# Kernel optimization log

Measured on AMD Instinct MI355X. Metric: run time of the kernel, lower is better.

The kernel has to match this reference:

```python
import jax, jax.numpy as jnp
import numpy as np
from jax import lax

EPS = 1e-10
NUM_ITERATIONS = 3  # init arg num_iterations
M, R = 16384, 32


def setup_inputs() -> dict:
    key = jax.random.key(0)
    x = jax.random.normal(key, (M, R, 2), dtype=jnp.float32)
    return {"x": x}


def reference(x):
    # x: (M, R, 2) -> complex (M, R); work with QT (R, M) so rows = columns
    r = x.shape[1]
    xc = (x[..., 0] + 1j * x[..., 1]).T  # (R, M) complex64
    idx = jnp.arange(r)

    # --- classical Gram-Schmidt pass (sequential over columns j) ---
    def gs_col(QT, j):
        def proj(v, i):
            qi = QT[i]
            coeff = jnp.sum(jnp.conj(qi) * v) * (i < j)  # only previous cols
            return v - coeff * qi, None
        v, _ = lax.scan(proj, xc[j], idx)
        v = v / jnp.sqrt(jnp.sum(jnp.abs(v) ** 2) + EPS)
        return QT.at[j].set(v), None

    QT, _ = lax.scan(gs_col, jnp.zeros_like(xc), idx)

    # --- iterative refinement sweeps: each column uses the OLD Q -> vmap over j ---
    def refine_col(QT, j):
        def proj(v, i):
            qi = QT[i]
            coeff = jnp.sum(jnp.conj(qi) * v) * (i != j)
            return v - 0.5 * coeff * qi, None
        v, _ = lax.scan(proj, QT[j], idx)
        return v / jnp.sqrt(jnp.sum(jnp.abs(v) ** 2) + EPS)

    for _ in range(NUM_ITERATIONS):
        QT = jax.vmap(refine_col, in_axes=(None, 0))(QT, idx)

    Q = QT.T  # (M, R)
    return jnp.stack([Q.real, Q.imag], axis=-1)
```

## Files before the change

kernel.cpp:

```cpp
#include <hip/hip_runtime.h>


#define M_ROWS 16384

__global__ __launch_bounds__(256) void gram_partial(const float* __restrict__ x,
                                                    float* __restrict__ G8) {
  __shared__ float lds[64 * 64];
  const int t = threadIdx.x;
  const int j = t & 31, g = t >> 5;
  const size_t row0 = (size_t)blockIdx.x * 64;
  float ar[4] = {0.f, 0.f, 0.f, 0.f};
  float ai[4] = {0.f, 0.f, 0.f, 0.f};
  const float4* src = (const float4*)(x + row0 * 64);
  float4* dst = (float4*)lds;
#pragma unroll
  for (int q = 0; q < 4; ++q) dst[t + 256 * q] = src[t + 256 * q];
  __syncthreads();
#pragma unroll 4
  for (int m = 0; m < 64; ++m) {
    const float2* row = (const float2*)(lds + m * 64);
    const float2 xj = row[j];
#pragma unroll
    for (int q = 0; q < 4; ++q) {
      const float2 xi = row[g + q * 8];
      ar[q] += xi.x * xj.x + xi.y * xj.y;
      ai[q] += xi.x * xj.y - xi.y * xj.x;
    }
  }
  float* P = G8 + (size_t)(blockIdx.x & 7) * 2048;
#pragma unroll
  for (int q = 0; q < 4; ++q) {
    const int i = g + q * 8;
    atomicAdd(&P[(i * 32 + j) * 2 + 0], ar[q]);
    atomicAdd(&P[(i * 32 + j) * 2 + 1], ai[q]);
  }
}

__global__ __launch_bounds__(64) void chol_solve(const float* __restrict__ x,
                                                 const float* __restrict__ G8,
                                                 float* __restrict__ out) {
  __shared__ float4 Gl[512];
  __shared__ float2 Acm[34 * 32];
  __shared__ float4 xsp[64 * 17];
  const int t = threadIdx.x;

  const float4* xp = (const float4*)(x + (size_t)blockIdx.x * 4096);
#pragma unroll
  for (int s = 0; s < 16; ++s) {
    const int g = t + 64 * s;
    xsp[(g >> 4) * 17 + (g & 15)] = xp[g];
  }
  const float4* G8f4 = (const float4*)G8;
#pragma unroll
  for (int s = 0; s < 8; ++s) {
    const int g = t + 64 * s;
    float4 acc = G8f4[g];
#pragma unroll
    for (int c = 1; c < 8; ++c) {
      const float4 p = G8f4[c * 512 + g];
      acc.x += p.x; acc.y += p.y; acc.z += p.z; acc.w += p.w;
    }
    Gl[g] = acc;
  }
  __syncthreads();

  if (t < 32) {
    const int j = t;
    float2 a[32];
#pragma unroll
    for (int i = 0; i < 32; ++i) a[i] = ((const float2*)Gl)[i * 32 + j];
#pragma unroll
    for (int k = 0; k < 31; ++k) {
      const float invd = 1.0f / __shfl(a[k].x, k);
      const float ux = a[k].x * invd;
      const float uy = a[k].y * invd;
      const bool act = (j > k);
#pragma unroll
      for (int i = k + 1; i < 32; ++i) {
        const float cr = __shfl(a[i].x, k);
        const float ci = __shfl(a[i].y, k);
        if (act) {
          a[i].x -= cr * ux - ci * uy;
          a[i].y -= cr * uy + ci * ux;
        }
      }
    }
#pragma unroll
    for (int i = 0; i < 32; ++i) Acm[j * 34 + i] = a[i];
  }
  __syncthreads();

  float2 xr[32];
#pragma unroll
  for (int q = 0; q < 16; ++q) {
    const float4 v = xsp[t * 17 + q];
    xr[2 * q].x = v.x; xr[2 * q].y = v.y;
    xr[2 * q + 1].x = v.z; xr[2 * q + 1].y = v.w;
  }
#pragma unroll
  for (int j = 0; j < 32; ++j) {
    const float d = Acm[j * 34 + j].x;
    const float invd = 1.0f / d;
    const float invs = 1.0f / sqrtf(d);
    const float2 u = {xr[j].x * invd, xr[j].y * invd};
    xr[j].x *= invs;
    xr[j].y *= invs;
#pragma unroll
    for (int i = j + 1; i < 32; ++i) {
      const float2 l = Acm[j * 34 + i];
      xr[i].x -= u.x * l.x + u.y * l.y;
      xr[i].y -= u.y * l.x - u.x * l.y;
    }
  }
#pragma unroll
  for (int q = 0; q < 16; ++q) {
    float4 v;
    v.x = xr[2 * q].x; v.y = xr[2 * q].y;
    v.z = xr[2 * q + 1].x; v.w = xr[2 * q + 1].y;
    xsp[t * 17 + q] = v;
  }
  __syncthreads();
  float4* op = (float4*)(out + (size_t)blockIdx.x * 4096);
#pragma unroll
  for (int s = 0; s < 16; ++s) {
    const int g = t + 64 * s;
    op[g] = xsp[(g >> 4) * 17 + (g & 15)];
  }
}

extern "C" void kernel_launch(void* const* d_in, const int* in_sizes, int n_in,
                              void* d_out, int out_size, void* d_ws, size_t ws_size,
                              hipStream_t stream) {
  const float* x = (const float*)d_in[0];
  float* out = (float*)d_out;
  float* G8 = (float*)d_ws;

  gram_partial<<<256, 256, 0, stream>>>(x, G8);
  chol_solve<<<256, 64, 0, stream>>>(x, G8, out);
}
```

Measured before the change: 101.6 us.

## Keep Cholesky factor in registers and broadcast via readlane instead of LDS

Every wavefront now runs the 32x32 complex factorization redundantly in registers and uses v_readlane broadcasts instead of __shfl. The forward solve reads the factor entries from registers through readlane, so the LDS staging of the factor, one barrier and the idle-thread branch are gone. Each thread also loads its x row straight from global into registers, skipping the LDS transpose on input. In exchange there is duplicated factorization work, heavier register pressure, and uncoalesced per-thread row loads.

After: 88.53 us. 12.9% less time.

```diff
diff --git a/kernel.cpp b/kernel.cpp
--- a/kernel.cpp
+++ b/kernel.cpp
@@ -2,6 +2,11 @@
 
 
 #define M_ROWS 16384
+
+__device__ __forceinline__ float rdlane(float v, int lane) {
+  return __builtin_bit_cast(
+      float, __builtin_amdgcn_readlane(__builtin_bit_cast(int, v), lane));
+}
 
 __global__ __launch_bounds__(256) void gram_partial(const float* __restrict__ x,
                                                     float* __restrict__ G8) {
@@ -40,16 +45,15 @@
                                                  const float* __restrict__ G8,
                                                  float* __restrict__ out) {
   __shared__ float4 Gl[512];
-  __shared__ float2 Acm[34 * 32];
   __shared__ float4 xsp[64 * 17];
   const int t = threadIdx.x;
+  const int j = t & 31;
 
-  const float4* xp = (const float4*)(x + (size_t)blockIdx.x * 4096);
+  const float4* xp = (const float4*)(x + ((size_t)blockIdx.x * 64 + t) * 64);
+  float4 xv[16];
 #pragma unroll
-  for (int s = 0; s < 16; ++s) {
-    const int g = t + 64 * s;
-    xsp[(g >> 4) * 17 + (g & 15)] = xp[g];
-  }
+  for (int q = 0; q < 16; ++q) xv[q] = xp[q];
+
   const float4* G8f4 = (const float4*)G8;
 #pragma unroll
   for (int s = 0; s < 8; ++s) {
@@ -64,54 +68,48 @@
   }
   __syncthreads();
 
-  if (t < 32) {
-    const int j = t;
-    float2 a[32];
+  float2 a[32];
 #pragma unroll
-    for (int i = 0; i < 32; ++i) a[i] = ((const float2*)Gl)[i * 32 + j];
+  for (int i = 0; i < 32; ++i) a[i] = ((const float2*)Gl)[i * 32 + j];
+
 #pragma unroll
-    for (int k = 0; k < 31; ++k) {
-      const float invd = 1.0f / __shfl(a[k].x, k);
-      const float ux = a[k].x * invd;
-      const float uy = a[k].y * invd;
-      const bool act = (j > k);
+  for (int k = 0; k < 31; ++k) {
+    const float invd = 1.0f / rdlane(a[k].x, k);
+    const bool act = (j > k);
+    const float ux = act ? a[k].x * invd : 0.0f;
+    const float uy = act ? a[k].y * invd : 0.0f;
 #pragma unroll
-      for (int i = k + 1; i < 32; ++i) {
-        const float cr = __shfl(a[i].x, k);
-        const float ci = __shfl(a[i].y, k);
-        if (act) {
-          a[i].x -= cr * ux - ci * uy;
-          a[i].y -= cr * uy + ci * ux;
-        }
-      }
+    for (int i = k + 1; i < 32; ++i) {
+      const float cr = rdlane(a[i].x, k);
+      const float ci = rdlane(a[i].y, k);
+      a[i].x -= cr * ux - ci * uy;
+      a[i].y -= cr * uy + ci * ux;
     }
-#pragma unroll
-    for (int i = 0; i < 32; ++i) Acm[j * 34 + i] = a[i];
   }
-  __syncthreads();
 
   float2 xr[32];
 #pragma unroll
   for (int q = 0; q < 16; ++q) {
-    const float4 v = xsp[t * 17 + q];
-    xr[2 * q].x = v.x; xr[2 * q].y = v.y;
-    xr[2 * q + 1].x = v.z; xr[2 * q + 1].y = v.w;
+    xr[2 * q].x = xv[q].x; xr[2 * q].y = xv[q].y;
+    xr[2 * q + 1].x = xv[q].z; xr[2 * q + 1].y = xv[q].w;
   }
 #pragma unroll
-  for (int j = 0; j < 32; ++j) {
-    const float d = Acm[j * 34 + j].x;
+  for (int jj = 0; jj < 32; ++jj) {
+    const float d = rdlane(a[jj].x, jj);
     const float invd = 1.0f / d;
     const float invs = 1.0f / sqrtf(d);
-    const float2 u = {xr[j].x * invd, xr[j].y * invd};
-    xr[j].x *= invs;
-    xr[j].y *= invs;
+    const float ux = xr[jj].x * invd, uy = xr[jj].y * invd;
+    xr[jj].x *= invs;
+    xr[jj].y *= invs;
 #pragma unroll
-    for (int i = j + 1; i < 32; ++i) {
-      const float2 l = Acm[j * 34 + i];
-      xr[i].x -= u.x * l.x + u.y * l.y;
-      xr[i].y -= u.y * l.x - u.x * l.y;
+    for (int i = jj + 1; i < 32; ++i) {
+      const float lr = rdlane(a[i].x, jj);
+      const float li = rdlane(a[i].y, jj);
+      xr[i].x -= ux * lr + uy * li;
+      xr[i].y -= uy * lr - ux * li;
     }
   }
+
 #pragma unroll
   for (int q = 0; q < 16; ++q) {
     float4 v;
```
